# Optimization experiments

Measured on AMD Instinct MI355X. Metric: run time of the kernel, lower is better.

The kernel has to match this reference:

```python
import jax, jax.numpy as jnp
import numpy as np

EPS = 1e-5
B, CIN, COUT, H, W, RED = 2, 64, 128, 256, 256, 8
K = 9  # 3x3 deformable kernel taps


def conv2d(x, w, b=None, pad=0):
    out = jax.lax.conv_general_dilated(x, w, (1, 1), [(pad, pad), (pad, pad)],
                                       dimension_numbers=('NCHW', 'OIHW', 'NCHW'))
    return out if b is None else out + b[None, :, None, None]


def batchnorm(x, g, b, m, v):
    s = g / jnp.sqrt(v + EPS)
    return x * s[None, :, None, None] + (b - m * s)[None, :, None, None]


def bilinear_sample(x, py, px):
    # x:(B,C,H,W), py/px:(B,K,H,W) float coords -> (B,C,K,H,W); zero outside bounds
    Bx, C, Hx, Wx = x.shape
    y0 = jnp.floor(py); x0 = jnp.floor(px)
    flat = x.reshape(Bx, C, Hx * Wx)

    def gather(yi, xi):
        valid = (yi >= 0) & (yi < Hx) & (xi >= 0) & (xi < Wx)
        idx = jnp.clip(yi, 0, Hx - 1) * Wx + jnp.clip(xi, 0, Wx - 1)
        g = jax.vmap(lambda f, i: jnp.take(f, i, axis=1))(flat, idx.reshape(Bx, -1))
        return g.reshape(Bx, C, *yi.shape[1:]) * valid[:, None].astype(x.dtype)

    wy1 = (py - y0)[:, None]; wy0 = 1.0 - wy1
    wx1 = (px - x0)[:, None]; wx0 = 1.0 - wx1
    y0i = y0.astype(jnp.int32); x0i = x0.astype(jnp.int32)
    return (gather(y0i, x0i) * wy0 * wx0 + gather(y0i, x0i + 1) * wy0 * wx1 +
            gather(y0i + 1, x0i) * wy1 * wx0 + gather(y0i + 1, x0i + 1) * wy1 * wx1)


def deform_conv(x, offsets, w, b):
    # torchvision DeformConv2d v1: offsets (B, 2*K, H, W), (dy,dx) per tap, row-major taps
    Bx, Cin, Hx, Wx = x.shape
    off = offsets.reshape(Bx, K, 2, Hx, Wx)
    ky, kx = jnp.meshgrid(jnp.arange(3), jnp.arange(3), indexing='ij')
    base_y = (jnp.arange(Hx)[None, :, None] + (ky.reshape(K) - 1)[:, None, None]).astype(x.dtype)  # (K,H,1)
    base_x = (jnp.arange(Wx)[None, None, :] + (kx.reshape(K) - 1)[:, None, None]).astype(x.dtype)  # (K,1,W)
    py = base_y[None] + off[:, :, 0]  # (B,K,H,W)
    px = base_x[None] + off[:, :, 1]
    sampled = bilinear_sample(x, py, px)  # (B,Cin,K,H,W)
    out = jnp.einsum('bckhw,ock->bohw', sampled, w.reshape(w.shape[0], Cin, K))
    return out + b[None, :, None, None]


def setup_inputs() -> dict:
    key = jax.random.key(0)
    ks = jax.random.split(key, 20)
    r = lambda i, shape, s=1.0: jax.random.normal(ks[i], shape, jnp.float32) * s
    cr = COUT // RED
    return dict(
        x=r(0, (B, CIN, H, W)),
        w_off=r(1, (2 * K, CIN, 3, 3), 0.04), b_off=jnp.zeros((2 * K,), jnp.float32),
        w_def=r(2, (COUT, CIN, 3, 3), 0.04), b_def=r(3, (COUT,), 0.01),
        bn_gamma=jnp.ones((COUT,), jnp.float32) + r(4, (COUT,), 0.1),
        bn_beta=r(5, (COUT,), 0.1),
        bn_mean=r(6, (COUT,), 0.1),
        bn_var=jax.random.uniform(ks[7], (COUT,), jnp.float32, 0.5, 1.5),
        se_w=r(8, (cr, COUT, 1, 1), 0.1), se_b=r(9, (cr,), 0.01),
        se_bn_gamma=jnp.ones((cr,), jnp.float32) + r(10, (cr,), 0.1),
        se_bn_beta=r(11, (cr,), 0.1),
        se_bn_mean=r(12, (cr,), 0.1),
        se_bn_var=jax.random.uniform(ks[13], (cr,), jnp.float32, 0.5, 1.5),
        phi=r(14, (cr, COUT), 0.3),
        ds_w=r(15, (COUT, CIN, 1, 1), 0.1),
        ds_bn_gamma=jnp.ones((COUT,), jnp.float32) + r(16, (COUT,), 0.1),
        ds_bn_beta=r(17, (COUT,), 0.1),
        ds_bn_mean=r(18, (COUT,), 0.1),
        ds_bn_var=jax.random.uniform(ks[19], (COUT,), jnp.float32, 0.5, 1.5),
    )


def reference(x, w_off, b_off, w_def, b_def, bn_gamma, bn_beta, bn_mean, bn_var,
              se_w, se_b, se_bn_gamma, se_bn_beta, se_bn_mean, se_bn_var, phi,
              ds_w, ds_bn_gamma, ds_bn_beta, ds_bn_mean, ds_bn_var):
    offsets = conv2d(x, w_off, b_off, pad=1)
    out = deform_conv(x, offsets, w_def, b_def)
    out = batchnorm(out, bn_gamma, bn_beta, bn_mean, bn_var)
    # DCSE: global-avg-pool -> 1x1 conv -> BN -> GELU -> matmul with softmax(phi) -> sigmoid gate
    pooled = out.mean(axis=(2, 3))  # (B,COUT)
    t = pooled @ se_w[:, :, 0, 0].T + se_b  # (B,COUT//RED)
    s = se_bn_gamma / jnp.sqrt(se_bn_var + EPS)
    t = jax.nn.gelu(t * s[None] + (se_bn_beta - se_bn_mean * s)[None], approximate=False)
    dw = jax.nn.sigmoid(t @ jax.nn.softmax(phi, axis=-1))  # (B,COUT)
    out = out * dw[:, :, None, None]
    identity = batchnorm(conv2d(x, ds_w), ds_bn_gamma, ds_bn_beta, ds_bn_mean, ds_bn_var)
    return jax.nn.relu(out + identity)
```

## Files before the change

kernel.cpp:

```cpp
#include <hip/hip_runtime.h>
#include <hip/hip_bf16.h>

typedef __hip_bfloat16 bf16;
typedef unsigned int u32;
typedef __attribute__((ext_vector_type(8))) short bf16x8;
typedef __attribute__((ext_vector_type(4))) float f32x4;

#define HHW 65536
#define SBH 584
#define SWU 292
#define REDW 132

__device__ __forceinline__ float b2f(bf16 v) { return __bfloat162float(v); }
__device__ __forceinline__ bf16  f2b(float v) { return __float2bfloat16(v); }
__device__ __forceinline__ float blo(u32 p) { return __uint_as_float(p << 16); }
__device__ __forceinline__ float bhi(u32 p) { return __uint_as_float(p & 0xffff0000u); }
__device__ __forceinline__ u32 pack2(float lo, float hi) {
    bf16 a = f2b(lo), c = f2b(hi);
    unsigned short ua, uc;
    __builtin_memcpy(&ua, &a, 2); __builtin_memcpy(&uc, &c, 2);
    return (u32)ua | ((u32)uc << 16);
}

__global__ __launch_bounds__(256) void k_prep(const float* __restrict__ x, bf16* __restrict__ xT,
        const float* __restrict__ w_off, const float* __restrict__ w_def, const float* __restrict__ b_def,
        const float* __restrict__ bng, const float* __restrict__ bnb, const float* __restrict__ bnm, const float* __restrict__ bnv,
        const float* __restrict__ ds_w, const float* __restrict__ dsg, const float* __restrict__ dsb,
        const float* __restrict__ dsm, const float* __restrict__ dsv,
        bf16* __restrict__ Wf, float* __restrict__ wloff, float* __restrict__ dws2,
        float* __restrict__ bnS, float* __restrict__ bnT2, float* __restrict__ dsT) {
    __shared__ bf16 tile[64][66];
    int g = blockIdx.x;
    int t = threadIdx.x;
    if (g < 2048) {
        int b = g >> 10;
        int pixbase = (g & 1023) << 6;
        int pix = t & 63, ci0 = t >> 6;
        const float* xb = x + ((size_t)b * 64) * HHW + pixbase + pix;
        for (int ci = ci0; ci < 64; ci += 4)
            tile[pix][ci] = f2b(xb[(size_t)ci * HHW]);
        __syncthreads();
        u32* dst32 = (u32*)(xT + ((size_t)b * HHW + pixbase) * 64);
        const u32* t32 = (const u32*)&tile[0][0];
        for (int i = t; i < 2048; i += 256) {
            int pix2 = i >> 5, j = i & 31;
            dst32[i] = t32[pix2 * 33 + j];
        }
        return;
    }
    int tid = (g - 2048) * 256 + t;
    for (int i = tid; i < 8 * 18 * 64 * 8; i += 8192) {
        int j = i & 7, lane = (i >> 3) & 63;
        int rem = i >> 9;
        int ks = rem % 18, ct = rem / 18;
        int co = ct * 16 + (lane & 15);
        int K  = ks * 32 + ((lane >> 4) << 3) + j;
        int ci = K & 63, kk = K >> 6;
        Wf[i] = f2b(w_def[co * 576 + ci * 9 + kk]);
    }
    for (int i = tid; i < 576 * 20; i += 8192) {
        int kci = i / 20, j = i - kci * 20;
        wloff[i] = (j < 18) ? w_off[j * 576 + kci] : 0.f;
    }
    if (tid < 8192) {
        int co = tid >> 6;
        float s2 = dsg[co] * rsqrtf(dsv[co] + 1e-5f);
        dws2[tid] = ds_w[tid] * s2;
    }
    if (tid < 128) {
        float s = bng[tid] * rsqrtf(bnv[tid] + 1e-5f);
        bnS[tid] = s;
        bnT2[tid] = (b_def[tid] - bnm[tid]) * s + bnb[tid];
        float s2 = dsg[tid] * rsqrtf(dsv[tid] + 1e-5f);
        dsT[tid] = dsb[tid] - dsm[tid] * s2;
    }
}

__global__ __launch_bounds__(256) void k_off(const float* __restrict__ x,
        const float* __restrict__ wloff, const float* __restrict__ b_off,
        u32* __restrict__ crec, uint2* __restrict__ wrec) {
    int g = blockIdx.x;
    int b = g >> 8, h = g & 255;
    int t = threadIdx.x;
    float acc[20];
    #pragma unroll
    for (int j = 0; j < 20; ++j) acc[j] = 0.f;
    const float* xb = x + ((size_t)b * 64) * HHW;
    for (int ci = 0; ci < 64; ++ci) {
        const float* xc = xb + (size_t)ci * HHW;
        #pragma unroll
        for (int ky = 0; ky < 3; ++ky) {
            int y = h + ky - 1;
            if ((unsigned)y >= 256u) continue;
            const float* row = xc + y * 256;
            float v0 = (t >= 1)   ? row[t - 1] : 0.f;
            float v1 = row[t];
            float v2 = (t <= 254) ? row[t + 1] : 0.f;
            const float4* wr = (const float4*)(wloff + (ci * 9 + ky * 3) * 20);
            #pragma unroll
            for (int q = 0; q < 5; ++q) {
                float4 wv = wr[q];
                acc[q*4+0] += v0 * wv.x; acc[q*4+1] += v0 * wv.y;
                acc[q*4+2] += v0 * wv.z; acc[q*4+3] += v0 * wv.w;
            }
            #pragma unroll
            for (int q = 0; q < 5; ++q) {
                float4 wv = wr[5 + q];
                acc[q*4+0] += v1 * wv.x; acc[q*4+1] += v1 * wv.y;
                acc[q*4+2] += v1 * wv.z; acc[q*4+3] += v1 * wv.w;
            }
            #pragma unroll
            for (int q = 0; q < 5; ++q) {
                float4 wv = wr[10 + q];
                acc[q*4+0] += v2 * wv.x; acc[q*4+1] += v2 * wv.y;
                acc[q*4+2] += v2 * wv.z; acc[q*4+3] += v2 * wv.w;
            }
        }
    }
    int tile = (h << 2) + (t >> 6);
    int pix  = t & 63;
    size_t rbase = ((size_t)(b * 1024 + tile)) * 576;
    #pragma unroll
    for (int k = 0; k < 9; ++k) {
        int ky = k / 3, kx = k - ky * 3;
        float dy = acc[2 * k]     + b_off[2 * k];
        float dx = acc[2 * k + 1] + b_off[2 * k + 1];
        float py = (float)(h + ky - 1) + dy;
        float px = (float)(t + kx - 1) + dx;
        float fy = floorf(py), fx = floorf(px);
        int y0 = (int)fy, x0 = (int)fx;
        float wy1 = py - fy, wx1 = px - fx;
        float wy0 = 1.f - wy1, wx0 = 1.f - wx1;
        int y1 = y0 + 1, x1 = x0 + 1;
        u32 yc0 = (u32)min(max(y0, 0), 255), yc1 = (u32)min(max(y1, 0), 255);
        u32 xc0 = (u32)min(max(x0, 0), 255), xc1 = (u32)min(max(x1, 0), 255);
        float m0 = ((unsigned)y0 < 256u) ? 1.f : 0.f;
        float m1 = ((unsigned)y1 < 256u) ? 1.f : 0.f;
        float n0 = ((unsigned)x0 < 256u) ? 1.f : 0.f;
        float n1 = ((unsigned)x1 < 256u) ? 1.f : 0.f;
        u32 c = yc0 | (xc0 << 8) | (yc1 << 16) | (xc1 << 24);
        uint2 wv;
        wv.x = pack2(wy0 * wx0 * m0 * n0, wy0 * wx1 * m0 * n1);
        wv.y = pack2(wy1 * wx0 * m1 * n0, wy1 * wx1 * m1 * n1);
        crec[rbase + k * 64 + pix] = c;
        wrec[rbase + k * 64 + pix] = wv;
    }
}

__global__ __launch_bounds__(512, 4) void k_deform(const bf16* __restrict__ xT,
        const u32* __restrict__ crec, const uint2* __restrict__ wrec,
        const bf16* __restrict__ Wf,
        const float* __restrict__ bnS, const float* __restrict__ bnT2,
        bf16* __restrict__ out_pre, float* __restrict__ part) {
    __shared__ bf16 smem[64 * SBH];
    int blk = blockIdx.x;
    int swz = (blk & 7) * 256 + (blk >> 3);
    int b = swz >> 10;
    int tile = swz & 1023;
    int pixbase = tile << 6;
    int t = threadIdx.x;
    int wid = t >> 6, l = t & 63;

    {
        int cig = l & 31, hf = l >> 5;
        size_t rbase = ((size_t)(b * 1024 + tile)) * 576;
        const u32*  crc = crec + rbase;
        const uint2* wrc = wrec + rbase;
        const u32* xw = (const u32*)xT + (size_t)b * (HHW * 32);
        u32* sw = (u32*)smem;
        int r = (wid << 1) + hf;
        u32  c0 = crc[r];
        uint2 w0 = wrc[r];
        #pragma unroll 6
        for (int it = 0; it < 36; ++it) {
            u32 c = c0; uint2 wv = w0;
            c0 = crc[r + 16]; w0 = wrc[r + 16];
            u32 y0 = c & 255u, x0 = (c >> 8) & 255u, y1 = (c >> 16) & 255u, x1 = c >> 24;
            u32 o00 = (y0 << 13) + (x0 << 5) + cig;
            u32 o01 = (y0 << 13) + (x1 << 5) + cig;
            u32 o10 = (y1 << 13) + (x0 << 5) + cig;
            u32 o11 = (y1 << 13) + (x1 << 5) + cig;
            u32 p00 = xw[o00], p01 = xw[o01], p10 = xw[o10], p11 = xw[o11];
            float w00 = blo(wv.x), w01 = bhi(wv.x), w10 = blo(wv.y), w11 = bhi(wv.y);
            float lo = blo(p00)*w00 + blo(p01)*w01 + blo(p10)*w10 + blo(p11)*w11;
            float hi = bhi(p00)*w00 + bhi(p01)*w01 + bhi(p10)*w10 + bhi(p11)*w11;
            int k9 = r >> 6, pix = r & 63;
            sw[pix * SWU + (k9 << 5) + cig] = pack2(lo, hi);
            r += 16;
        }
    }
    __syncthreads();

    int pxg = wid >> 1, coh = wid & 1;
    int wp = pxg << 4;
    int lr = l & 15, lg = l >> 4;
    f32x4 acc[4];
    #pragma unroll
    for (int ct = 0; ct < 4; ++ct) acc[ct] = (f32x4){0.f, 0.f, 0.f, 0.f};
    const bf16* arow = smem + (wp + lr) * SBH + lg * 8;
    const bf16* wbase = Wf + l * 8;
    #pragma unroll
    for (int ks = 0; ks < 18; ++ks) {
        bf16x8 af = *(const bf16x8*)(arow + ks * 32);
        #pragma unroll
        for (int ct = 0; ct < 4; ++ct) {
            int cti = coh * 4 + ct;
            bf16x8 bfr = *(const bf16x8*)(wbase + (cti * 18 + ks) * 512);
            acc[ct] = __builtin_amdgcn_mfma_f32_16x16x32_bf16(af, bfr, acc[ct], 0, 0, 0);
        }
    }
    __syncthreads();
    float* red = (float*)smem;
    #pragma unroll
    for (int ct = 0; ct < 4; ++ct) {
        int co = (coh * 4 + ct) * 16 + lr;
        float sc = bnS[co], sh = bnT2[co];
        #pragma unroll
        for (int r = 0; r < 4; ++r) {
            int m = lg * 4 + r;
            red[(wp + m) * REDW + co] = acc[ct][r] * sc + sh;
        }
    }
    __syncthreads();
    bf16* op = out_pre + ((size_t)b * HHW + pixbase) * 128;
    for (int i = t; i < 8192; i += 512)
        op[i] = f2b(red[(i >> 7) * REDW + (i & 127)]);
    if (t < 128) {
        float sum = 0.f;
        #pragma unroll
        for (int p = 0; p < 64; ++p) sum += red[p * REDW + t];
        part[((size_t)(b * 128 + t)) * 1024 + tile] = sum;
    }
}

__global__ __launch_bounds__(256) void k_pool(const float* __restrict__ part, float* __restrict__ pooled) {
    int bco = blockIdx.x;
    int t = threadIdx.x;
    const float* p = part + (size_t)bco * 1024;
    float sum = 0.f;
    for (int i = t; i < 1024; i += 256) sum += p[i];
    __shared__ float r[256];
    r[t] = sum; __syncthreads();
    for (int ofs = 128; ofs > 0; ofs >>= 1) {
        if (t < ofs) r[t] += r[t + ofs];
        __syncthreads();
    }
    if (t == 0) pooled[bco] = r[0] * (1.f / 65536.f);
}

__global__ __launch_bounds__(256) void k_se(const float* __restrict__ pooled,
        const float* __restrict__ se_w, const float* __restrict__ se_b,
        const float* __restrict__ sg_, const float* __restrict__ sb_,
        const float* __restrict__ sm_, const float* __restrict__ sv_,
        const float* __restrict__ phi, float* __restrict__ dw) {
    __shared__ float tl[32];
    __shared__ float sp[16][128];
    __shared__ float pl[256];
    int t = threadIdx.x;
    pl[t] = pooled[t];
    __syncthreads();
    if (t < 32) {
        int b = t >> 4, r = t & 15;
        float d = se_b[r];
        for (int c = 0; c < 128; ++c) d += pl[b * 128 + c] * se_w[r * 128 + c];
        float s = sg_[r] * rsqrtf(sv_[r] + 1e-5f);
        float xb = d * s + (sb_[r] - sm_[r] * s);
        tl[t] = 0.5f * xb * (1.f + erff(xb * 0.70710678118654752f));
    }
    if (t >= 32 && t < 48) {
        int r = t - 32;
        float m = -1e30f;
        for (int c = 0; c < 128; ++c) m = fmaxf(m, phi[r * 128 + c]);
        float ssum = 0.f;
        for (int c = 0; c < 128; ++c) { float e = expf(phi[r * 128 + c] - m); sp[r][c] = e; ssum += e; }
        float inv = 1.f / ssum;
        for (int c = 0; c < 128; ++c) sp[r][c] *= inv;
    }
    __syncthreads();
    {
        int b = t >> 7, co = t & 127;
        float a = 0.f;
        #pragma unroll
        for (int r = 0; r < 16; ++r) a += tl[b * 16 + r] * sp[r][co];
        dw[t] = 1.f / (1.f + expf(-a));
    }
}

__global__ __launch_bounds__(256) void k_final(const bf16* __restrict__ xT,
        const bf16* __restrict__ out_pre, const float* __restrict__ dws2,
        const float* __restrict__ dsT, const float* __restrict__ dw,
        float* __restrict__ out) {
    __shared__ float xtile[64 * 68];
    __shared__ float otile[64 * 129];
    __shared__ float dwl[128], dsTl[128];
    int g = blockIdx.x;
    int b = g >> 10;
    int pixbase = (g & 1023) << 6;
    int t = threadIdx.x;
    const bf16* xp = xT + ((size_t)b * HHW + pixbase) * 64;
    for (int i = t; i < 4096; i += 256)
        xtile[(i >> 6) * 68 + (i & 63)] = b2f(xp[i]);
    if (t < 128) { dwl[t] = dw[b * 128 + t]; dsTl[t] = dsT[t]; }
    __syncthreads();
    int co = t >> 1, half = t & 1;
    float4 wr[16];
    const float4* wp = (const float4*)(dws2 + co * 64);
    #pragma unroll
    for (int i = 0; i < 16; ++i) wr[i] = wp[i];
    float dwv = dwl[co], dst = dsTl[co];
    const bf16* opp = out_pre + ((size_t)b * HHW + pixbase) * 128 + co;
    for (int p0 = 0; p0 < 32; ++p0) {
        int p = half * 32 + p0;
        const float* xr = xtile + p * 68;
        float a = 0.f;
        #pragma unroll
        for (int i = 0; i < 16; ++i) {
            float4 xv = *(const float4*)(xr + i * 4);
            a += xv.x * wr[i].x + xv.y * wr[i].y + xv.z * wr[i].z + xv.w * wr[i].w;
        }
        float opre = b2f(opp[(size_t)p * 128]);
        float v = opre * dwv + a + dst;
        otile[p * 129 + co] = fmaxf(v, 0.f);
    }
    __syncthreads();
    float* ob = out + (size_t)b * 128 * HHW + pixbase;
    for (int i = t; i < 8192; i += 256) {
        int cco = i >> 6, pp = i & 63;
        ob[(size_t)cco * HHW + pp] = otile[pp * 129 + cco];
    }
}

extern "C" void kernel_launch(void* const* d_in, const int* in_sizes, int n_in,
                              void* d_out, int out_size, void* d_ws, size_t ws_size,
                              hipStream_t stream) {
    const float* x     = (const float*)d_in[0];
    const float* w_off = (const float*)d_in[1];
    const float* b_off = (const float*)d_in[2];
    const float* w_def = (const float*)d_in[3];
    const float* b_def = (const float*)d_in[4];
    const float* bng   = (const float*)d_in[5];
    const float* bnb   = (const float*)d_in[6];
    const float* bnm   = (const float*)d_in[7];
    const float* bnv   = (const float*)d_in[8];
    const float* se_w  = (const float*)d_in[9];
    const float* se_b  = (const float*)d_in[10];
    const float* sbg   = (const float*)d_in[11];
    const float* sbb   = (const float*)d_in[12];
    const float* sbm   = (const float*)d_in[13];
    const float* sbv   = (const float*)d_in[14];
    const float* phi   = (const float*)d_in[15];
    const float* ds_w  = (const float*)d_in[16];
    const float* dsg   = (const float*)d_in[17];
    const float* dsb   = (const float*)d_in[18];
    const float* dsm   = (const float*)d_in[19];
    const float* dsv   = (const float*)d_in[20];
    float* out = (float*)d_out;

    char* w = (char*)d_ws;
    bf16*  xT     = (bf16*)w;   w += 16777216;
    bf16*  Wf     = (bf16*)w;   w += 147456;
    float* wloff  = (float*)w;  w += 46080;
    float* dws2   = (float*)w;  w += 32768;
    float* bnS    = (float*)w;  w += 512;
    float* bnT2   = (float*)w;  w += 512;
    float* dsT    = (float*)w;  w += 512;
    bf16*  opre   = (bf16*)w;   w += 33554432;
    float* part   = (float*)w;  w += 1048576;
    float* pooled = (float*)w;  w += 1024;
    float* dwv    = (float*)w;  w += 1024;
    u32*   crec   = (u32*)w;    w += 4720896;
    uint2* wrec   = (uint2*)w;  w += 9441792;

    hipLaunchKernelGGL(k_prep, dim3(2080), dim3(256), 0, stream, x, xT, w_off, w_def, b_def,
                       bng, bnb, bnm, bnv, ds_w, dsg, dsb, dsm, dsv,
                       Wf, wloff, dws2, bnS, bnT2, dsT);
    hipLaunchKernelGGL(k_off, dim3(512), dim3(256), 0, stream, x, wloff, b_off, crec, wrec);
    hipLaunchKernelGGL(k_deform, dim3(2048), dim3(512), 0, stream, xT, crec, wrec, Wf, bnS, bnT2, opre, part);
    hipLaunchKernelGGL(k_pool, dim3(256), dim3(256), 0, stream, part, pooled);
    hipLaunchKernelGGL(k_se, dim3(1), dim3(256), 0, stream, pooled, se_w, se_b, sbg, sbb, sbm, sbv, phi, dwv);
    hipLaunchKernelGGL(k_final, dim3(2048), dim3(256), 0, stream, xT, opre, dws2, dsT, dwv, out);
}
```

Baseline: 422.5 us.

## Fuse offset conv into deform kernel using bf16 MFMA and LDS sampling records

Removes the separate fp32 scalar offset-convolution kernel. The offset 3x3 conv is now computed inside the deform kernel as a bf16 MFMA implicit GEMM over the channel-last xT tensor. The per-tap coordinate and bilinear-weight records are built in LDS instead of being written to and re-read from global memory. This cuts one launch and roughly 14 MB of global traffic, and replaces scalar FMAs with matrix instructions. In exchange, offsets are computed in bf16, which lowers precision and can shift sampling positions. It also adds LDS, extra barriers and some redundant MFMA work, since 32 output columns are padded for 18 offsets.

```diff
diff --git a/kernel.cpp b/kernel.cpp
--- a/kernel.cpp
+++ b/kernel.cpp
@@ -10,6 +10,7 @@
 #define SBH 584
 #define SWU 292
 #define REDW 132
+#define SOFF_W 20
 
 __device__ __forceinline__ float b2f(bf16 v) { return __bfloat162float(v); }
 __device__ __forceinline__ bf16  f2b(float v) { return __float2bfloat16(v); }
@@ -27,7 +28,7 @@
         const float* __restrict__ bng, const float* __restrict__ bnb, const float* __restrict__ bnm, const float* __restrict__ bnv,
         const float* __restrict__ ds_w, const float* __restrict__ dsg, const float* __restrict__ dsb,
         const float* __restrict__ dsm, const float* __restrict__ dsv,
-        bf16* __restrict__ Wf, float* __restrict__ wloff, float* __restrict__ dws2,
+        bf16* __restrict__ Wf, bf16* __restrict__ Woff_f, float* __restrict__ dws2,
         float* __restrict__ bnS, float* __restrict__ bnT2, float* __restrict__ dsT) {
     __shared__ bf16 tile[64][66];
     int g = blockIdx.x;
@@ -58,9 +59,14 @@
         int ci = K & 63, kk = K >> 6;
         Wf[i] = f2b(w_def[co * 576 + ci * 9 + kk]);
     }
-    for (int i = tid; i < 576 * 20; i += 8192) {
-        int kci = i / 20, j = i - kci * 20;
-        wloff[i] = (j < 18) ? w_off[j * 576 + kci] : 0.f;
+    for (int i = tid; i < 2 * 18 * 64 * 8; i += 8192) {
+        int j = i & 7, lane = (i >> 3) & 63;
+        int rem = i >> 9;
+        int ks = rem % 18, ct = rem / 18;
+        int co = ct * 16 + (lane & 15);
+        int K  = ks * 32 + ((lane >> 4) << 3) + j;
+        int ci = K & 63, kk = K >> 6;
+        Woff_f[i] = (co < 18) ? f2b(w_off[co * 576 + ci * 9 + kk]) : f2b(0.f);
     }
     if (tid < 8192) {
         int co = tid >> 6;
@@ -76,105 +82,94 @@
     }
 }
 
-__global__ __launch_bounds__(256) void k_off(const float* __restrict__ x,
-        const float* __restrict__ wloff, const float* __restrict__ b_off,
-        u32* __restrict__ crec, uint2* __restrict__ wrec) {
-    int g = blockIdx.x;
-    int b = g >> 8, h = g & 255;
-    int t = threadIdx.x;
-    float acc[20];
-    #pragma unroll
-    for (int j = 0; j < 20; ++j) acc[j] = 0.f;
-    const float* xb = x + ((size_t)b * 64) * HHW;
-    for (int ci = 0; ci < 64; ++ci) {
-        const float* xc = xb + (size_t)ci * HHW;
-        #pragma unroll
-        for (int ky = 0; ky < 3; ++ky) {
-            int y = h + ky - 1;
-            if ((unsigned)y >= 256u) continue;
-            const float* row = xc + y * 256;
-            float v0 = (t >= 1)   ? row[t - 1] : 0.f;
-            float v1 = row[t];
-            float v2 = (t <= 254) ? row[t + 1] : 0.f;
-            const float4* wr = (const float4*)(wloff + (ci * 9 + ky * 3) * 20);
-            #pragma unroll
-            for (int q = 0; q < 5; ++q) {
-                float4 wv = wr[q];
-                acc[q*4+0] += v0 * wv.x; acc[q*4+1] += v0 * wv.y;
-                acc[q*4+2] += v0 * wv.z; acc[q*4+3] += v0 * wv.w;
-            }
-            #pragma unroll
-            for (int q = 0; q < 5; ++q) {
-                float4 wv = wr[5 + q];
-                acc[q*4+0] += v1 * wv.x; acc[q*4+1] += v1 * wv.y;
-                acc[q*4+2] += v1 * wv.z; acc[q*4+3] += v1 * wv.w;
-            }
-            #pragma unroll
-            for (int q = 0; q < 5; ++q) {
-                float4 wv = wr[10 + q];
-                acc[q*4+0] += v2 * wv.x; acc[q*4+1] += v2 * wv.y;
-                acc[q*4+2] += v2 * wv.z; acc[q*4+3] += v2 * wv.w;
-            }
-        }
-    }
-    int tile = (h << 2) + (t >> 6);
-    int pix  = t & 63;
-    size_t rbase = ((size_t)(b * 1024 + tile)) * 576;
-    #pragma unroll
-    for (int k = 0; k < 9; ++k) {
-        int ky = k / 3, kx = k - ky * 3;
-        float dy = acc[2 * k]     + b_off[2 * k];
-        float dx = acc[2 * k + 1] + b_off[2 * k + 1];
-        float py = (float)(h + ky - 1) + dy;
-        float px = (float)(t + kx - 1) + dx;
-        float fy = floorf(py), fx = floorf(px);
-        int y0 = (int)fy, x0 = (int)fx;
-        float wy1 = py - fy, wx1 = px - fx;
-        float wy0 = 1.f - wy1, wx0 = 1.f - wx1;
-        int y1 = y0 + 1, x1 = x0 + 1;
-        u32 yc0 = (u32)min(max(y0, 0), 255), yc1 = (u32)min(max(y1, 0), 255);
-        u32 xc0 = (u32)min(max(x0, 0), 255), xc1 = (u32)min(max(x1, 0), 255);
-        float m0 = ((unsigned)y0 < 256u) ? 1.f : 0.f;
-        float m1 = ((unsigned)y1 < 256u) ? 1.f : 0.f;
-        float n0 = ((unsigned)x0 < 256u) ? 1.f : 0.f;
-        float n1 = ((unsigned)x1 < 256u) ? 1.f : 0.f;
-        u32 c = yc0 | (xc0 << 8) | (yc1 << 16) | (xc1 << 24);
-        uint2 wv;
-        wv.x = pack2(wy0 * wx0 * m0 * n0, wy0 * wx1 * m0 * n1);
-        wv.y = pack2(wy1 * wx0 * m1 * n0, wy1 * wx1 * m1 * n1);
-        crec[rbase + k * 64 + pix] = c;
-        wrec[rbase + k * 64 + pix] = wv;
-    }
-}
-
 __global__ __launch_bounds__(512, 4) void k_deform(const bf16* __restrict__ xT,
-        const u32* __restrict__ crec, const uint2* __restrict__ wrec,
+        const bf16* __restrict__ Woff_f, const float* __restrict__ b_off,
         const bf16* __restrict__ Wf,
         const float* __restrict__ bnS, const float* __restrict__ bnT2,
         bf16* __restrict__ out_pre, float* __restrict__ part) {
-    __shared__ bf16 smem[64 * SBH];
+    __shared__ bf16 smem[64 * SBH + 2304 + 1152];
+    uint2* wrl = (uint2*)(smem + 64 * SBH);
+    u32*   crl = (u32*)(smem + 64 * SBH + 2304);
     int blk = blockIdx.x;
     int swz = (blk & 7) * 256 + (blk >> 3);
     int b = swz >> 10;
     int tile = swz & 1023;
     int pixbase = tile << 6;
+    int h = pixbase >> 8;
+    int w0 = pixbase & 255;
     int t = threadIdx.x;
     int wid = t >> 6, l = t & 63;
+    int lr = l & 15, lg = l >> 4;
+
+    {
+        int pxg0 = wid & 3, ct0 = wid >> 2;
+        int pix = pxg0 * 16 + lr;
+        const bf16* xb = xT + (size_t)b * HHW * 64;
+        f32x4 oacc = (f32x4){0.f, 0.f, 0.f, 0.f};
+        #pragma unroll
+        for (int ks = 0; ks < 18; ++ks) {
+            int K0 = ks * 32 + lg * 8;
+            int k9 = K0 >> 6, ci0 = K0 & 63;
+            int ky = k9 / 3, kx = k9 - 3 * ky;
+            int py = h + ky - 1;
+            int px = w0 + pix + kx - 1;
+            bf16x8 af = {0, 0, 0, 0, 0, 0, 0, 0};
+            if ((unsigned)py < 256u && (unsigned)px < 256u)
+                af = *(const bf16x8*)(xb + ((size_t)(py * 256 + px)) * 64 + ci0);
+            bf16x8 bfr = *(const bf16x8*)(Woff_f + ((ct0 * 18 + ks) * 64 + l) * 8);
+            oacc = __builtin_amdgcn_mfma_f32_16x16x32_bf16(af, bfr, oacc, 0, 0, 0);
+        }
+        float* offs_lds = (float*)smem;
+        int co = ct0 * 16 + lr;
+        if (co < 18) {
+            float bo = b_off[co];
+            #pragma unroll
+            for (int r = 0; r < 4; ++r) {
+                int m = pxg0 * 16 + lg * 4 + r;
+                offs_lds[m * SOFF_W + co] = oacc[r] + bo;
+            }
+        }
+    }
+    __syncthreads();
+
+    {
+        const float* offs_lds = (const float*)smem;
+        for (int r = t; r < 576; r += 512) {
+            int pix = r & 63, k = r >> 6;
+            int ky = k / 3, kx = k - 3 * ky;
+            float dy = offs_lds[pix * SOFF_W + 2 * k];
+            float dx = offs_lds[pix * SOFF_W + 2 * k + 1];
+            float py = (float)(h + ky - 1) + dy;
+            float px = (float)(w0 + pix + kx - 1) + dx;
+            float fy = floorf(py), fx = floorf(px);
+            int y0 = (int)fy, x0 = (int)fx;
+            float wy1 = py - fy, wx1 = px - fx;
+            float wy0 = 1.f - wy1, wx0 = 1.f - wx1;
+            int y1 = y0 + 1, x1 = x0 + 1;
+            u32 yc0 = (u32)min(max(y0, 0), 255), yc1 = (u32)min(max(y1, 0), 255);
+            u32 xc0 = (u32)min(max(x0, 0), 255), xc1 = (u32)min(max(x1, 0), 255);
+            float m0 = ((unsigned)y0 < 256u) ? 1.f : 0.f;
+            float m1 = ((unsigned)y1 < 256u) ? 1.f : 0.f;
+            float n0 = ((unsigned)x0 < 256u) ? 1.f : 0.f;
+            float n1 = ((unsigned)x1 < 256u) ? 1.f : 0.f;
+            crl[r] = yc0 | (xc0 << 8) | (yc1 << 16) | (xc1 << 24);
+            uint2 wv;
+            wv.x = pack2(wy0 * wx0 * m0 * n0, wy0 * wx1 * m0 * n1);
+            wv.y = pack2(wy1 * wx0 * m1 * n0, wy1 * wx1 * m1 * n1);
+            wrl[r] = wv;
+        }
+    }
+    __syncthreads();
 
     {
         int cig = l & 31, hf = l >> 5;
-        size_t rbase = ((size_t)(b * 1024 + tile)) * 576;
-        const u32*  crc = crec + rbase;
-        const uint2* wrc = wrec + rbase;
         const u32* xw = (const u32*)xT + (size_t)b * (HHW * 32);
         u32* sw = (u32*)smem;
-        int r = (wid << 1) + hf;
-        u32  c0 = crc[r];
-        uint2 w0 = wrc[r];
-        #pragma unroll 6
+        #pragma unroll 4
         for (int it = 0; it < 36; ++it) {
-            u32 c = c0; uint2 wv = w0;
-            c0 = crc[r + 16]; w0 = wrc[r + 16];
+            int r = it * 16 + (wid << 1) + hf;
+            u32 c = crl[r];
+            uint2 wv = wrl[r];
             u32 y0 = c & 255u, x0 = (c >> 8) & 255u, y1 = (c >> 16) & 255u, x1 = c >> 24;
             u32 o00 = (y0 << 13) + (x0 << 5) + cig;
             u32 o01 = (y0 << 13) + (x1 << 5) + cig;
@@ -186,14 +181,12 @@
             float hi = bhi(p00)*w00 + bhi(p01)*w01 + bhi(p10)*w10 + bhi(p11)*w11;
             int k9 = r >> 6, pix = r & 63;
             sw[pix * SWU + (k9 << 5) + cig] = pack2(lo, hi);
-            r += 16;
         }
     }
     __syncthreads();
 
     int pxg = wid >> 1, coh = wid & 1;
     int wp = pxg << 4;
-    int lr = l & 15, lg = l >> 4;
     f32x4 acc[4];
     #pragma unroll
     for (int ct = 0; ct < 4; ++ct) acc[ct] = (f32x4){0.f, 0.f, 0.f, 0.f};
@@ -359,7 +352,7 @@
     char* w = (char*)d_ws;
     bf16*  xT     = (bf16*)w;   w += 16777216;
     bf16*  Wf     = (bf16*)w;   w += 147456;
-    float* wloff  = (float*)w;  w += 46080;
+    bf16*  Woff_f = (bf16*)w;   w += 36864;
     float* dws2   = (float*)w;  w += 32768;
     float* bnS    = (float*)w;  w += 512;
     float* bnT2   = (float*)w;  w += 512;
@@ -368,14 +361,11 @@
     float* part   = (float*)w;  w += 1048576;
     float* pooled = (float*)w;  w += 1024;
     float* dwv    = (float*)w;  w += 1024;
-    u32*   crec   = (u32*)w;    w += 4720896;
-    uint2* wrec   = (uint2*)w;  w += 9441792;
 
     hipLaunchKernelGGL(k_prep, dim3(2080), dim3(256), 0, stream, x, xT, w_off, w_def, b_def,
                        bng, bnb, bnm, bnv, ds_w, dsg, dsb, dsm, dsv,
-                       Wf, wloff, dws2, bnS, bnT2, dsT);
-    hipLaunchKernelGGL(k_off, dim3(512), dim3(256), 0, stream, x, wloff, b_off, crec, wrec);
-    hipLaunchKernelGGL(k_deform, dim3(2048), dim3(512), 0, stream, xT, crec, wrec, Wf, bnS, bnT2, opre, part);
+                       Wf, Woff_f, dws2, bnS, bnT2, dsT);
+    hipLaunchKernelGGL(k_deform, dim3(2048), dim3(512), 0, stream, xT, Woff_f, b_off, Wf, bnS, bnT2, opre, part);
     hipLaunchKernelGGL(k_pool, dim3(256), dim3(256), 0, stream, part, pooled);
     hipLaunchKernelGGL(k_se, dim3(1), dim3(256), 0, stream, pooled, se_w, se_b, sbg, sbb, sbm, sbv, phi, dwv);
     hipLaunchKernelGGL(k_final, dim3(2048), dim3(256), 0, stream, xT, opre, dws2, dsT, dwv, out);
```

After: 360.6 us. 14.7% less time.
